# Kernel tuning notes

Hardware: AMD Instinct MI355X
Metric: run time of the kernel (lower is better)

## Reference

```python
import jax, jax.numpy as jnp
import numpy as np

N_NODES = 50000
HIDDEN = 256
DEPTH = 6
NUM_GRAPHS = 500


def _build_graph(n):
    # 4-regular directed graph: node i -> (i+1, i-1, i+5, i-5) mod n.
    offs = np.array([1, -1, 5, -5], dtype=np.int64)
    src = np.repeat(np.arange(n, dtype=np.int64), 4)
    dst = (src + np.tile(offs, n)) % n
    # incoming edge ids of node u (edge id = 4*src + offset_index)
    u = np.arange(n, dtype=np.int64)
    incoming = np.stack([4 * ((u - 1) % n) + 0,
                         4 * ((u + 1) % n) + 1,
                         4 * ((u - 5) % n) + 2,
                         4 * ((u + 5) % n) + 3], axis=1)  # [n,4]
    E = 4 * n
    pred = incoming[src]           # [E,4] candidate line-graph predecessors of edge e
    pred_src = pred // 4           # source node of each predecessor edge
    keep = pred_src != dst[:, None]  # drop backtracking edge (exactly 1 per row)
    lg_src = pred[keep]                                   # [3E]
    lg_dst = np.repeat(np.arange(E, dtype=np.int64), 4)[keep.ravel()]  # [3E]
    return src, dst, lg_src, lg_dst


def setup_inputs() -> dict:
    key = jax.random.key(0)
    ks = jax.random.split(key, 8)
    n, H = N_NODES, HIDDEN
    E = 4 * n
    _, dst, lg_src, lg_dst = _build_graph(n)
    graph_ids = np.arange(n, dtype=np.int64) // (n // NUM_GRAPHS)
    s = 0.02  # small weight scale keeps relu message passing stable over DEPTH iters
    return {
        "x_nodes": jax.random.normal(ks[0], (n, 35), jnp.float32),
        "x_edges": jax.random.normal(ks[1], (E, 40), jnp.float32),
        "t_m": jax.random.normal(ks[2], (E, H), jnp.float32) * 0.1,
        "W_i": jax.random.normal(ks[3], (40, H), jnp.float32) * s,
        "W_h": jax.random.normal(ks[4], (H, H), jnp.float32) * s,
        "W_o": jax.random.normal(ks[5], (35 + H, H), jnp.float32) * s,
        "b_o": jax.random.normal(ks[6], (H,), jnp.float32) * s,
        "edge_dst": jnp.asarray(dst, jnp.int32),
        "lg_src": jnp.asarray(lg_src, jnp.int32),
        "lg_dst": jnp.asarray(lg_dst, jnp.int32),
        "graph_ids": jnp.asarray(graph_ids, jnp.int32),
        "num_graphs": NUM_GRAPHS,
    }


def reference(x_nodes, x_edges, t_m, W_i, W_h, W_o, b_o,
              edge_dst, lg_src, lg_dst, graph_ids, num_graphs):
    E = x_edges.shape[0]
    n = x_nodes.shape[0]
    binput = x_edges @ W_i                       # W_i has no bias
    g_m = jax.nn.relu(binput)                    # [E,H] per-edge message
    # tree-message aggregation over line graph is constant across depth iters
    t_agg = jax.ops.segment_sum(t_m[lg_src], lg_dst, num_segments=E)
    for _ in range(DEPTH - 1):
        g_agg = jax.ops.segment_sum(g_m[lg_src], lg_dst, num_segments=E)
        g_m = jax.nn.relu(binput + (g_agg + t_agg) @ W_h)
    # edge -> dst-node aggregation (copy_e + sum)
    nei1 = jax.ops.segment_sum(g_m, edge_dst, num_segments=n)
    nei2 = jax.ops.segment_sum(t_m, edge_dst, num_segments=n)
    ainput = jnp.concatenate([x_nodes, nei1 + nei2], axis=1)  # [n, 35+H]
    atom_hiddens = jax.nn.relu(ainput @ W_o + b_o)
    # dgl.mean_nodes: per-graph mean of node features
    sums = jax.ops.segment_sum(atom_hiddens, graph_ids, num_segments=num_graphs)
    counts = jax.ops.segment_sum(jnp.ones((n, 1), atom_hiddens.dtype), graph_ids,
                                 num_segments=num_graphs)
    return sums / counts
```

## Files before the change

### kernel.cpp

```cpp
#include <hip/hip_runtime.h>


#define H 256

typedef __attribute__((ext_vector_type(4))) float f32x4;
typedef __attribute__((ext_vector_type(8))) short bf16x8;

#define MFMA(a, b, c) __builtin_amdgcn_mfma_f32_16x16x32_bf16((a), (b), (c), 0, 0, 0)

__device__ __forceinline__ float bf2f(ushort u) {
  union { unsigned int i; float f; } v; v.i = ((unsigned int)u) << 16; return v.f;
}
__device__ __forceinline__ ushort f2bf(float f) {
  union { float f; unsigned int i; } v; v.f = f;
  unsigned int i = v.i;
  i += 0x7fffu + ((i >> 16) & 1u);
  return (ushort)(i >> 16);
}

union AFrag { bf16x8 v; ushort u[8]; };

__device__ __forceinline__ int edge_delta(int o) {
  return ((o & 2) ? 5 : 1) * ((o & 1) ? -1 : 1);
}

__global__ __launch_bounds__(256) void prep_weights_kernel(
    const float* __restrict__ Wh, const float* __restrict__ Wi, const float* __restrict__ Wo,
    ushort* __restrict__ WhT_swz, ushort* __restrict__ WiT,
    ushort* __restrict__ WoT1, ushort* __restrict__ WoT2) {
  const int nn = blockIdx.x;
  const int t = threadIdx.x;
  WhT_swz[nn * H + (t ^ ((nn & 7) << 3))] = f2bf(Wh[t * H + nn]);
  WoT2[nn * H + t] = f2bf(Wo[(35 + t) * H + nn]);
  if (t < 64) {
    WiT[nn * 64 + t] = (t < 40) ? f2bf(Wi[t * H + nn]) : (ushort)0;
    WoT1[nn * 64 + t] = (t < 35) ? f2bf(Wo[t * H + nn]) : (ushort)0;
  }
}

__global__ __launch_bounds__(256) void sum_tm_kernel(
    const float* __restrict__ t_m, ushort* __restrict__ t3, ushort* __restrict__ t4,
    int n, int useT4) {
  const int idx = blockIdx.x * 256 + threadIdx.x;
  const int s = idx >> 5;
  if (s >= n) return;
  const int cg = (idx & 31) * 8;
  int im1 = s - 1; if (im1 < 0) im1 += n;
  int ip1 = s + 1; if (ip1 >= n) ip1 -= n;
  int im5 = s - 5; if (im5 < 0) im5 += n;
  int ip5 = s + 5; if (ip5 >= n) ip5 -= n;
  const size_t e0 = (size_t)(4 * im1 + 0) * H + cg;
  const size_t e1 = (size_t)(4 * ip1 + 1) * H + cg;
  const size_t e2 = (size_t)(4 * im5 + 2) * H + cg;
  const size_t e3 = (size_t)(4 * ip5 + 3) * H + cg;
  f32x4 v0a = *(const f32x4*)(t_m + e0), v0b = *(const f32x4*)(t_m + e0 + 4);
  f32x4 v1a = *(const f32x4*)(t_m + e1), v1b = *(const f32x4*)(t_m + e1 + 4);
  f32x4 v2a = *(const f32x4*)(t_m + e2), v2b = *(const f32x4*)(t_m + e2 + 4);
  f32x4 v3a = *(const f32x4*)(t_m + e3), v3b = *(const f32x4*)(t_m + e3 + 4);
  f32x4 Sa = v0a + v1a + v2a + v3a;
  f32x4 Sb = v0b + v1b + v2b + v3b;
  f32x4 ra[4] = {Sa - v1a, Sa - v0a, Sa - v3a, Sa - v2a};
  f32x4 rb[4] = {Sb - v1b, Sb - v0b, Sb - v3b, Sb - v2b};
#pragma unroll
  for (int o = 0; o < 4; ++o) {
    AFrag a;
#pragma unroll
    for (int i = 0; i < 4; ++i) { a.u[i] = f2bf(ra[o][i]); a.u[4 + i] = f2bf(rb[o][i]); }
    *(bf16x8*)(t3 + (size_t)(4 * s + o) * H + cg) = a.v;
  }
  if (useT4) {
    AFrag a;
#pragma unroll
    for (int i = 0; i < 4; ++i) { a.u[i] = f2bf(Sa[i]); a.u[4 + i] = f2bf(Sb[i]); }
    *(bf16x8*)(t4 + (size_t)s * H + cg) = a.v;
  }
}

__global__ __launch_bounds__(512, 4) void prologue_kernel(
    const float* __restrict__ x_edges, const ushort* __restrict__ t3,
    const ushort* __restrict__ WhT_swz, const ushort* __restrict__ WiT,
    ushort* __restrict__ tb, ushort* __restrict__ g0P, int E, int n) {
  extern __shared__ ushort lds[];
  const int tid = threadIdx.x;
  const int wid = tid >> 6, lane = tid & 63, l15 = lane & 15, kg = lane >> 4;
  const int ch = blockIdx.x >> 8;
  const int colbase = ch << 7;

  {
    const bf16x8* src = (const bf16x8*)(WhT_swz + (size_t)colbase * H);
    bf16x8* dstl = (bf16x8*)lds;
#pragma unroll
    for (int j = 0; j < 8; ++j) dstl[tid + j * 512] = src[tid + j * 512];
  }
  __syncthreads();

  const int nchunks = (E + 127) >> 7;
  for (int c = blockIdx.x & 255; c < nchunks; c += 256) {
    const int row0 = (c << 7) + wid * 16;
    if (row0 >= E) continue;
    const int r = row0 + l15;

    f32x4 acc[8];
#pragma unroll
    for (int i = 0; i < 8; ++i) acc[i] = (f32x4){0.f, 0.f, 0.f, 0.f};

#pragma unroll
    for (int ks = 0; ks < 2; ++ks) {
      const int k = ks * 32 + kg * 8;
      AFrag a;
      if (k < 40) {
        const float* xp = x_edges + (size_t)r * 40 + k;
        f32x4 x0 = *(const f32x4*)(xp);
        f32x4 x1 = *(const f32x4*)(xp + 4);
#pragma unroll
        for (int i = 0; i < 4; ++i) { a.u[i] = f2bf(x0[i]); a.u[4 + i] = f2bf(x1[i]); }
      } else {
#pragma unroll
        for (int i = 0; i < 8; ++i) a.u[i] = 0;
      }
#pragma unroll
      for (int nf = 0; nf < 8; ++nf) {
        const int col = colbase + nf * 16 + l15;
        bf16x8 b = *(const bf16x8*)(WiT + col * 64 + k);
        acc[nf] = MFMA(a.v, b, acc[nf]);
      }
    }

    int rout[4];
#pragma unroll
    for (int j = 0; j < 4; ++j) {
      const int er = row0 + kg * 4 + j;
      const int sw = er >> 2, ow = er & 3;
      int d = sw + edge_delta(ow);
      if (d < 0) d += n; else if (d >= n) d -= n;
      rout[j] = 4 * d + ow;
    }

#pragma unroll
    for (int nf = 0; nf < 8; ++nf) {
      const int col = colbase + nf * 16 + l15;
#pragma unroll
      for (int j = 0; j < 4; ++j)
        g0P[(size_t)rout[j] * H + col] = f2bf(fmaxf(acc[nf][j], 0.f));
    }

#pragma unroll
    for (int ks = 0; ks < 8; ++ks) {
      const int k = ks * 32 + kg * 8;
      bf16x8 av = *(const bf16x8*)(t3 + (size_t)r * H + k);
#pragma unroll
      for (int nf = 0; nf < 8; ++nf) {
        const int colloc = nf * 16 + l15;
        bf16x8 b = *(const bf16x8*)(lds + colloc * H + (k ^ ((colloc & 7) << 3)));
        acc[nf] = MFMA(av, b, acc[nf]);
      }
    }

#pragma unroll
    for (int nf = 0; nf < 8; ++nf) {
      const int col = colbase + nf * 16 + l15;
#pragma unroll
      for (int j = 0; j < 4; ++j)
        tb[(size_t)(row0 + kg * 4 + j) * H + col] = f2bf(acc[nf][j]);
    }
  }
}

__global__ __launch_bounds__(512, 4) void mp_iter_kernel(
    const ushort* __restrict__ gOldP, const ushort* __restrict__ tb,
    const ushort* __restrict__ WhT_swz, ushort* __restrict__ gNewP, int E, int n) {
  extern __shared__ ushort lds[];
  const int tid = threadIdx.x;
  const int wid = tid >> 6, lane = tid & 63, l15 = lane & 15, kg = lane >> 4;
  const int ch = blockIdx.x >> 8;
  const int colbase = ch << 7;

  {
    const bf16x8* src = (const bf16x8*)(WhT_swz + (size_t)colbase * H);
    bf16x8* dstl = (bf16x8*)lds;
#pragma unroll
    for (int j = 0; j < 8; ++j) dstl[tid + j * 512] = src[tid + j * 512];
  }
  __syncthreads();

  const int nchunks = (E + 127) >> 7;
  for (int c = blockIdx.x & 255; c < nchunks; c += 256) {
    const int row0 = (c << 7) + wid * 16;
    if (row0 >= E) continue;
    const int r = row0 + l15;
    const int s = r >> 2, o = r & 3, drop = o ^ 1;
    const int a0 = (drop == 0) ? 1 : 0;
    const int a1 = 1 + (drop <= 1);
    const int a2 = 2 + (drop <= 2);
    const ushort* b0 = gOldP + (size_t)(4 * s + a0) * H;
    const ushort* b1 = gOldP + (size_t)(4 * s + a1) * H;
    const ushort* b2 = gOldP + (size_t)(4 * s + a2) * H;

    f32x4 acc[8];
#pragma unroll
    for (int i = 0; i < 8; ++i) acc[i] = (f32x4){0.f, 0.f, 0.f, 0.f};

#pragma unroll
    for (int ks = 0; ks < 8; ++ks) {
      const int k = ks * 32 + kg * 8;
      bf16x8 av0 = *(const bf16x8*)(b0 + k);
      bf16x8 av1 = *(const bf16x8*)(b1 + k);
      bf16x8 av2 = *(const bf16x8*)(b2 + k);
#pragma unroll
      for (int nf = 0; nf < 8; ++nf) {
        const int colloc = nf * 16 + l15;
        bf16x8 b = *(const bf16x8*)(lds + colloc * H + (k ^ ((colloc & 7) << 3)));
        f32x4 t = MFMA(av0, b, acc[nf]);
        t = MFMA(av1, b, t);
        acc[nf] = MFMA(av2, b, t);
      }
    }

    int rout[4];
#pragma unroll
    for (int j = 0; j < 4; ++j) {
      const int er = row0 + kg * 4 + j;
      const int sw = er >> 2, ow = er & 3;
      int d = sw + edge_delta(ow);
      if (d < 0) d += n; else if (d >= n) d -= n;
      rout[j] = 4 * d + ow;
    }

#pragma unroll
    for (int nf = 0; nf < 8; ++nf) {
      const int col = colbase + nf * 16 + l15;
#pragma unroll
      for (int j = 0; j < 4; ++j) {
        const float v = bf2f(tb[(size_t)(row0 + kg * 4 + j) * H + col]) + acc[nf][j];
        gNewP[(size_t)rout[j] * H + col] = f2bf(fmaxf(v, 0.f));
      }
    }
  }
}

__global__ __launch_bounds__(256) void readout_kernel(
    const float* __restrict__ x_nodes, const float* __restrict__ t_m,
    const ushort* __restrict__ gP, const ushort* __restrict__ t4,
    const float* __restrict__ b_o,
    const ushort* __restrict__ WoT1, const ushort* __restrict__ WoT2,
    float* __restrict__ out, int n, int npg, int useT4) {
  const int gidx = blockIdx.x;
  const int wid = threadIdx.x >> 6;
  const int lane = threadIdx.x & 63;
  const int l15 = lane & 15;
  const int kg = lane >> 4;
  const int u0 = gidx * npg;

  __shared__ float red[H];

  f32x4 acc[2][16];
#pragma unroll
  for (int m = 0; m < 2; ++m)
#pragma unroll
    for (int i = 0; i < 16; ++i) acc[m][i] = (f32x4){0.f, 0.f, 0.f, 0.f};

  int uu[2]; bool mv[2]; int inc[2][4];
#pragma unroll
  for (int m = 0; m < 2; ++m) {
    const int mf = wid * 2 + m;
    const int rl = mf * 16 + l15;
    mv[m] = rl < npg;
    const int u = u0 + rl;
    uu[m] = u;
    if (mv[m]) {
      inc[m][0] = 4 * ((u - 1 + n) % n);
      inc[m][1] = 4 * ((u + 1) % n) + 1;
      inc[m][2] = 4 * ((u - 5 + n) % n) + 2;
      inc[m][3] = 4 * ((u + 5) % n) + 3;
    } else {
      inc[m][0] = inc[m][1] = inc[m][2] = inc[m][3] = 0;
    }
  }

#pragma unroll
  for (int ks = 0; ks < 2; ++ks) {
    const int k = ks * 32 + kg * 8;
#pragma unroll
    for (int m = 0; m < 2; ++m) {
      AFrag a;
#pragma unroll
      for (int i = 0; i < 8; ++i) {
        const int kk = k + i;
        a.u[i] = (mv[m] && kk < 35) ? f2bf(x_nodes[(size_t)uu[m] * 35 + kk]) : (ushort)0;
      }
#pragma unroll
      for (int nf = 0; nf < 16; ++nf) {
        bf16x8 b = *(const bf16x8*)(WoT1 + (nf * 16 + l15) * 64 + k);
        acc[m][nf] = MFMA(a.v, b, acc[m][nf]);
      }
    }
  }

#pragma unroll
  for (int ks = 0; ks < 8; ++ks) {
    const int k = ks * 32 + kg * 8;
#pragma unroll
    for (int m = 0; m < 2; ++m) {
      AFrag a;
      if (mv[m]) {
        float s[8];
#pragma unroll
        for (int i = 0; i < 8; ++i) s[i] = 0.f;
        const int e4 = 4 * uu[m];
#pragma unroll
        for (int j = 0; j < 4; ++j) {
          bf16x8 gv = *(const bf16x8*)(gP + (size_t)(e4 + j) * H + k);
#pragma unroll
          for (int i = 0; i < 8; ++i) s[i] += bf2f((ushort)gv[i]);
        }
        if (useT4) {
          bf16x8 tv = *(const bf16x8*)(t4 + (size_t)uu[m] * H + k);
#pragma unroll
          for (int i = 0; i < 8; ++i) s[i] += bf2f((ushort)tv[i]);
        } else {
#pragma unroll
          for (int j = 0; j < 4; ++j) {
            const float* tp = t_m + (size_t)inc[m][j] * H + k;
            f32x4 t0 = *(const f32x4*)tp;
            f32x4 t1 = *(const f32x4*)(tp + 4);
#pragma unroll
            for (int i = 0; i < 4; ++i) { s[i] += t0[i]; s[4 + i] += t1[i]; }
          }
        }
#pragma unroll
        for (int i = 0; i < 8; ++i) a.u[i] = f2bf(s[i]);
      } else {
#pragma unroll
        for (int i = 0; i < 8; ++i) a.u[i] = 0;
      }
#pragma unroll
      for (int nf = 0; nf < 16; ++nf) {
        bf16x8 b = *(const bf16x8*)(WoT2 + (nf * 16 + l15) * H + k);
        acc[m][nf] = MFMA(a.v, b, acc[m][nf]);
      }
    }
  }

  red[threadIdx.x] = 0.f;
  __syncthreads();

#pragma unroll
  for (int nf = 0; nf < 16; ++nf) {
    const int col = nf * 16 + l15;
    const float bias = b_o[col];
    float cs = 0.f;
#pragma unroll
    for (int m = 0; m < 2; ++m) {
#pragma unroll
      for (int j = 0; j < 4; ++j) {
        const int rr = (wid * 2 + m) * 16 + kg * 4 + j;
        if (rr < npg) cs += fmaxf(acc[m][nf][j] + bias, 0.f);
      }
    }
    cs += __shfl_xor(cs, 16);
    cs += __shfl_xor(cs, 32);
    if (kg == 0) atomicAdd(&red[col], cs);
  }
  __syncthreads();
  out[(size_t)gidx * H + threadIdx.x] = red[threadIdx.x] * (1.0f / (float)npg);
}

extern "C" void kernel_launch(void* const* d_in, const int* in_sizes, int n_in,
                              void* d_out, int out_size, void* d_ws, size_t ws_size,
                              hipStream_t stream) {
  const float* x_nodes = (const float*)d_in[0];
  const float* x_edges = (const float*)d_in[1];
  const float* t_m     = (const float*)d_in[2];
  const float* W_i     = (const float*)d_in[3];
  const float* W_h     = (const float*)d_in[4];
  const float* W_o     = (const float*)d_in[5];
  const float* b_o     = (const float*)d_in[6];
  (void)n_in;

  const int n = in_sizes[0] / 35;
  const int E = in_sizes[1] / 40;
  const int num_graphs = out_size / H;
  const int npg = n / num_graphs;

  char* ws = (char*)d_ws;
  ushort* WhT_swz = (ushort*)(ws);
  ushort* WiT  = (ushort*)(ws + 131072);
  ushort* WoT1 = (ushort*)(ws + 164 * 1024);
  ushort* WoT2 = (ushort*)(ws + 200 * 1024);
  size_t off = 336 * 1024;
  const size_t gbytes = (size_t)E * H * 2;
  ushort* tb = (ushort*)(ws + off); off += gbytes;
  ushort* gA = (ushort*)(ws + off); off += gbytes;
  ushort* gB = (ushort*)(ws + off); off += gbytes;
  ushort* t3 = gB;
  const size_t t4bytes = (size_t)n * H * 2;
  const int useT4 = (ws_size >= off + t4bytes) ? 1 : 0;
  ushort* t4 = (ushort*)(ws + off);

  prep_weights_kernel<<<256, 256, 0, stream>>>(W_h, W_i, W_o, WhT_swz, WiT, WoT1, WoT2);
  sum_tm_kernel<<<(n * 32 + 255) / 256, 256, 0, stream>>>(t_m, t3, t4, n, useT4);
  prologue_kernel<<<512, 512, 65536, stream>>>(x_edges, t3, WhT_swz, WiT, tb, gA, E, n);

  ushort* src = gA;
  ushort* dst = gB;
  for (int it = 0; it < 5; ++it) {
    mp_iter_kernel<<<512, 512, 65536, stream>>>(src, tb, WhT_swz, dst, E, n);
    ushort* tmp = src; src = dst; dst = tmp;
  }

  readout_kernel<<<num_graphs, 256, 0, stream>>>(x_nodes, t_m, src, t4, b_o, WoT1, WoT2,
                                                 (float*)d_out, n, npg, useT4);
}
```

Baseline: 790.2 us.

## Transpose MFMA operands and permute weight columns for vectorized 16-byte row stores

Swaps the A and B operands of the MFMAs so each lane's accumulator holds consecutive output columns of one row. The weight columns are permuted (phi) in the prep kernel so the packed results land contiguously. Output rows are then written as 16-byte bf16x8 stores instead of scattered 2-byte stores, and the tb reads in mp_iter become vector loads. The A-operand row loads are also prefetched one k-step ahead in mp_iter, and the t3 loads are hoisted in the init kernel, which raises register pressure.

```diff
diff --git a/kernel.cpp b/kernel.cpp
--- a/kernel.cpp
+++ b/kernel.cpp
@@ -22,6 +22,10 @@
 
 __device__ __forceinline__ int edge_delta(int o) {
   return ((o & 2) ? 5 : 1) * ((o & 1) ? -1 : 1);
+}
+
+__device__ __forceinline__ int phi(int L) {
+  return (L & ~31) | (((L >> 2) & 1) << 4) | (((L >> 3) & 3) << 2) | (L & 3);
 }
 
 __global__ __launch_bounds__(256) void prep_weights_kernel(
@@ -30,10 +34,11 @@
     ushort* __restrict__ WoT1, ushort* __restrict__ WoT2) {
   const int nn = blockIdx.x;
   const int t = threadIdx.x;
-  WhT_swz[nn * H + (t ^ ((nn & 7) << 3))] = f2bf(Wh[t * H + nn]);
+  const int w = phi(nn);
+  WhT_swz[w * H + (t ^ ((w & 7) << 3))] = f2bf(Wh[t * H + nn]);
   WoT2[nn * H + t] = f2bf(Wo[(35 + t) * H + nn]);
   if (t < 64) {
-    WiT[nn * 64 + t] = (t < 40) ? f2bf(Wi[t * H + nn]) : (ushort)0;
+    WiT[w * 64 + t] = (t < 40) ? f2bf(Wi[t * H + nn]) : (ushort)0;
     WoT1[nn * 64 + t] = (t < 35) ? f2bf(Wo[t * H + nn]) : (ushort)0;
   }
 }
@@ -100,68 +105,76 @@
     if (row0 >= E) continue;
     const int r = row0 + l15;
 
+    const float* xp = x_edges + (size_t)r * 40;
+    f32x4 xa0 = *(const f32x4*)(xp + kg * 8);
+    f32x4 xa1 = *(const f32x4*)(xp + kg * 8 + 4);
+    f32x4 xb0, xb1;
+    if (kg == 0) { xb0 = *(const f32x4*)(xp + 32); xb1 = *(const f32x4*)(xp + 36); }
+
+    bf16x8 av[8];
+#pragma unroll
+    for (int ks = 0; ks < 8; ++ks)
+      av[ks] = *(const bf16x8*)(t3 + (size_t)r * H + ks * 32 + kg * 8);
+
     f32x4 acc[8];
 #pragma unroll
     for (int i = 0; i < 8; ++i) acc[i] = (f32x4){0.f, 0.f, 0.f, 0.f};
 
-#pragma unroll
-    for (int ks = 0; ks < 2; ++ks) {
-      const int k = ks * 32 + kg * 8;
-      AFrag a;
-      if (k < 40) {
-        const float* xp = x_edges + (size_t)r * 40 + k;
-        f32x4 x0 = *(const f32x4*)(xp);
-        f32x4 x1 = *(const f32x4*)(xp + 4);
-#pragma unroll
-        for (int i = 0; i < 4; ++i) { a.u[i] = f2bf(x0[i]); a.u[4 + i] = f2bf(x1[i]); }
-      } else {
-#pragma unroll
-        for (int i = 0; i < 8; ++i) a.u[i] = 0;
-      }
-#pragma unroll
-      for (int nf = 0; nf < 8; ++nf) {
-        const int col = colbase + nf * 16 + l15;
-        bf16x8 b = *(const bf16x8*)(WiT + col * 64 + k);
-        acc[nf] = MFMA(a.v, b, acc[nf]);
-      }
-    }
-
-    int rout[4];
-#pragma unroll
-    for (int j = 0; j < 4; ++j) {
-      const int er = row0 + kg * 4 + j;
-      const int sw = er >> 2, ow = er & 3;
-      int d = sw + edge_delta(ow);
-      if (d < 0) d += n; else if (d >= n) d -= n;
-      rout[j] = 4 * d + ow;
-    }
-
+    AFrag bx0, bx1;
+#pragma unroll
+    for (int i = 0; i < 4; ++i) { bx0.u[i] = f2bf(xa0[i]); bx0.u[4 + i] = f2bf(xa1[i]); }
+    if (kg == 0) {
+#pragma unroll
+      for (int i = 0; i < 4; ++i) { bx1.u[i] = f2bf(xb0[i]); bx1.u[4 + i] = f2bf(xb1[i]); }
+    } else {
+#pragma unroll
+      for (int i = 0; i < 8; ++i) bx1.u[i] = 0;
+    }
 #pragma unroll
     for (int nf = 0; nf < 8; ++nf) {
-      const int col = colbase + nf * 16 + l15;
-#pragma unroll
-      for (int j = 0; j < 4; ++j)
-        g0P[(size_t)rout[j] * H + col] = f2bf(fmaxf(acc[nf][j], 0.f));
+      const int w = colbase + nf * 16 + l15;
+      bf16x8 a0 = *(const bf16x8*)(WiT + w * 64 + kg * 8);
+      acc[nf] = MFMA(a0, bx0.v, acc[nf]);
+      bf16x8 a1 = *(const bf16x8*)(WiT + w * 64 + 32 + kg * 8);
+      acc[nf] = MFMA(a1, bx1.v, acc[nf]);
+    }
+
+    const int s_ = r >> 2, o_ = r & 3;
+    int d_ = s_ + edge_delta(o_);
+    if (d_ < 0) d_ += n; else if (d_ >= n) d_ -= n;
+    ushort* gout = g0P + (size_t)(4 * d_ + o_) * H + colbase + kg * 8;
+#pragma unroll
+    for (int tt = 0; tt < 4; ++tt) {
+      AFrag pk;
+#pragma unroll
+      for (int i = 0; i < 4; ++i) {
+        pk.u[i]     = f2bf(fmaxf(acc[2 * tt][i], 0.f));
+        pk.u[4 + i] = f2bf(fmaxf(acc[2 * tt + 1][i], 0.f));
+      }
+      *(bf16x8*)(gout + tt * 32) = pk.v;
     }
 
 #pragma unroll
     for (int ks = 0; ks < 8; ++ks) {
       const int k = ks * 32 + kg * 8;
-      bf16x8 av = *(const bf16x8*)(t3 + (size_t)r * H + k);
 #pragma unroll
       for (int nf = 0; nf < 8; ++nf) {
         const int colloc = nf * 16 + l15;
-        bf16x8 b = *(const bf16x8*)(lds + colloc * H + (k ^ ((colloc & 7) << 3)));
-        acc[nf] = MFMA(av, b, acc[nf]);
-      }
-    }
-
-#pragma unroll
-    for (int nf = 0; nf < 8; ++nf) {
-      const int col = colbase + nf * 16 + l15;
-#pragma unroll
-      for (int j = 0; j < 4; ++j)
-        tb[(size_t)(row0 + kg * 4 + j) * H + col] = f2bf(acc[nf][j]);
+        bf16x8 a = *(const bf16x8*)(lds + colloc * H + (k ^ ((colloc & 7) << 3)));
+        acc[nf] = MFMA(a, av[ks], acc[nf]);
+      }
+    }
+
+    ushort* tbp = tb + (size_t)r * H + colbase + kg * 8;
+#pragma unroll
+    for (int tt = 0; tt < 4; ++tt) {
+      AFrag pk;
+#pragma unroll
+      for (int i = 0; i < 4; ++i) {
+        pk.u[i]     = f2bf(acc[2 * tt][i]);
+        pk.u[4 + i] = f2bf(acc[2 * tt + 1][i]);
+      }
+      *(bf16x8*)(tbp + tt * 32) = pk.v;
     }
   }
 }
@@ -192,9 +205,19 @@
     const int a0 = (drop == 0) ? 1 : 0;
     const int a1 = 1 + (drop <= 1);
     const int a2 = 2 + (drop <= 2);
-    const ushort* b0 = gOldP + (size_t)(4 * s + a0) * H;
-    const ushort* b1 = gOldP + (size_t)(4 * s + a1) * H;
-    const ushort* b2 = gOldP + (size_t)(4 * s + a2) * H;
+    const ushort* b0 = gOldP + (size_t)(4 * s + a0) * H + kg * 8;
+    const ushort* b1 = gOldP + (size_t)(4 * s + a1) * H + kg * 8;
+    const ushort* b2 = gOldP + (size_t)(4 * s + a2) * H + kg * 8;
+
+    bf16x8 tbv[4];
+    const ushort* tbp = tb + (size_t)r * H + colbase + kg * 8;
+#pragma unroll
+    for (int tt = 0; tt < 4; ++tt) tbv[tt] = *(const bf16x8*)(tbp + tt * 32);
+
+    bf16x8 p0[2], p1[2], p2[2];
+    p0[0] = *(const bf16x8*)(b0);
+    p1[0] = *(const bf16x8*)(b1);
+    p2[0] = *(const bf16x8*)(b2);
 
     f32x4 acc[8];
 #pragma unroll
@@ -202,38 +225,38 @@
 
 #pragma unroll
     for (int ks = 0; ks < 8; ++ks) {
+      const int cur = ks & 1, nxt = cur ^ 1;
+      if (ks < 7) {
+        const int k2 = (ks + 1) * 32;
+        p0[nxt] = *(const bf16x8*)(b0 + k2);
+        p1[nxt] = *(const bf16x8*)(b1 + k2);
+        p2[nxt] = *(const bf16x8*)(b2 + k2);
+      }
       const int k = ks * 32 + kg * 8;
-      bf16x8 av0 = *(const bf16x8*)(b0 + k);
-      bf16x8 av1 = *(const bf16x8*)(b1 + k);
-      bf16x8 av2 = *(const bf16x8*)(b2 + k);
 #pragma unroll
       for (int nf = 0; nf < 8; ++nf) {
         const int colloc = nf * 16 + l15;
-        bf16x8 b = *(const bf16x8*)(lds + colloc * H + (k ^ ((colloc & 7) << 3)));
-        f32x4 t = MFMA(av0, b, acc[nf]);
-        t = MFMA(av1, b, t);
-        acc[nf] = MFMA(av2, b, t);
-      }
-    }
-
-    int rout[4];
-#pragma unroll
-    for (int j = 0; j < 4; ++j) {
-      const int er = row0 + kg * 4 + j;
-      const int sw = er >> 2, ow = er & 3;
-      int d = sw + edge_delta(ow);
-      if (d < 0) d += n; else if (d >= n) d -= n;
-      rout[j] = 4 * d + ow;
-    }
-
-#pragma unroll
-    for (int nf = 0; nf < 8; ++nf) {
-      const int col = colbase + nf * 16 + l15;
-#pragma unroll
-      for (int j = 0; j < 4; ++j) {
-        const float v = bf2f(tb[(size_t)(row0 + kg * 4 + j) * H + col]) + acc[nf][j];
-        gNewP[(size_t)rout[j] * H + col] = f2bf(fmaxf(v, 0.f));
-      }
+        bf16x8 a = *(const bf16x8*)(lds + colloc * H + (k ^ ((colloc & 7) << 3)));
+        f32x4 u = MFMA(a, p0[cur], acc[nf]);
+        u = MFMA(a, p1[cur], u);
+        acc[nf] = MFMA(a, p2[cur], u);
+      }
+    }
+
+    int d = s + edge_delta(o);
+    if (d < 0) d += n; else if (d >= n) d -= n;
+    ushort* gout = gNewP + (size_t)(4 * d + o) * H + colbase + kg * 8;
+#pragma unroll
+    for (int tt = 0; tt < 4; ++tt) {
+      AFrag pk;
+#pragma unroll
+      for (int i = 0; i < 4; ++i) {
+        float v0 = bf2f((ushort)tbv[tt][i])     + acc[2 * tt][i];
+        float v1 = bf2f((ushort)tbv[tt][4 + i]) + acc[2 * tt + 1][i];
+        pk.u[i]     = f2bf(fmaxf(v0, 0.f));
+        pk.u[4 + i] = f2bf(fmaxf(v1, 0.f));
+      }
+      *(bf16x8*)(gout + tt * 32) = pk.v;
     }
   }
 }
```

New measurement: 746.0 us. -5.6%, faster.
